# Kernel tuning notes

Measured on AMD Instinct MI355X. Metric: run time of the kernel, lower is better.

## Reference

```python
import jax, jax.numpy as jnp
import numpy as np

B, HF, WF = 4, 64, 64   # fine (output) resolution
HC, WC = 32, 32         # coarse resolution
CF = 256                # fine channels
CC = 256                # coarse channels (DCN input)
F = 256                 # filters
DG, K, KK = 8, 3, 9     # deformable groups, kernel
OFFS = DG * 2 * KK      # 144 offset channels
MASKS = DG * KK         # 72 mask channels
PAD = 1                 # 'same' padding for k=3, dil=1


def setup_inputs() -> dict:
    key = jax.random.key(0)
    ks = jax.random.split(key, 8)
    rn = lambda k, s, sc: jax.random.normal(k, s, jnp.float32) * sc
    return {
        "fine": rn(ks[0], (B, HF, WF, CF), 1.0),
        "coarse": rn(ks[1], (B, HC, WC, CC), 1.0),
        "fs_attn_w": rn(ks[2], (CF, CF), (2.0 / CF) ** 0.5),
        "fs_conv_w": rn(ks[3], (CF, F), (2.0 / CF) ** 0.5),
        "offset_w": rn(ks[4], (F + CC, 2 * F), (2.0 / (F + CC)) ** 0.5),
        "om_w": rn(ks[5], (K, K, 2 * F, OFFS + MASKS), 0.01),  # original is zero-init; small random for nontrivial offsets
        "om_b": jnp.zeros((OFFS + MASKS,), jnp.float32),
        "dcn_kernel": rn(ks[6], (KK * CC, F), 1.0 / np.sqrt(KK * CC)),
        "dcn_bias": jnp.zeros((F,), jnp.float32),
    }


def _dcn_columns(x, offset, mask):
    # x: [B,H,W,C]; offset: [B,H,W,DG,KK,2] (dy,dx); mask: [B,H,W,DG,KK]
    Bx, H, W, C = x.shape
    Cg = C // DG
    xg = x.reshape(Bx, H, W, DG, Cg)
    dt = x.dtype
    ky, kx = jnp.meshgrid(jnp.arange(K), jnp.arange(K), indexing="ij")
    tap_y = (ky.reshape(-1) - PAD).astype(dt)  # [KK]
    tap_x = (kx.reshape(-1) - PAD).astype(dt)
    # fractional sample positions, stride 1 / dilation 1
    py = (jnp.arange(H, dtype=dt)[None, :, None, None, None]
          + tap_y[None, None, None, None, :] + offset[..., 0])  # [B,H,W,DG,KK]
    px = (jnp.arange(W, dtype=dt)[None, None, :, None, None]
          + tap_x[None, None, None, None, :] + offset[..., 1])
    y0 = jnp.floor(py); x0 = jnp.floor(px)
    wy1 = py - y0; wx1 = px - x0
    wy0 = 1.0 - wy1; wx0 = 1.0 - wx1
    y0i = y0.astype(jnp.int32); x0i = x0.astype(jnp.int32)
    bi = jnp.arange(Bx).reshape(Bx, 1, 1, 1, 1)
    gi = jnp.arange(DG).reshape(1, 1, 1, DG, 1)

    def gather(yi, xi):
        valid = (yi >= 0) & (yi < H) & (xi >= 0) & (xi < W)
        yc = jnp.clip(yi, 0, H - 1)
        xc = jnp.clip(xi, 0, W - 1)
        v = xg[bi, yc, xc, gi]  # [B,H,W,DG,KK,Cg]
        return v * valid.astype(dt)[..., None]

    val = (gather(y0i, x0i) * (wy0 * wx0)[..., None]
           + gather(y0i, x0i + 1) * (wy0 * wx1)[..., None]
           + gather(y0i + 1, x0i) * (wy1 * wx0)[..., None]
           + gather(y0i + 1, x0i + 1) * (wy1 * wx1)[..., None])
    val = val * mask[..., None]  # modulation
    # column layout: tap-major, then channel (g*Cg + cg), matching kernel [KK*C, F]
    cols = jnp.transpose(val, (0, 1, 2, 4, 3, 5)).reshape(Bx, H, W, KK * C)
    return cols


def reference(fine, coarse, fs_attn_w, fs_conv_w, offset_w, om_w, om_b,
              dcn_kernel, dcn_bias):
    # 1) upsample coarse to fine resolution (half-pixel bilinear)
    coarse_up = jax.image.resize(coarse, (B, HF, WF, CC), "bilinear")
    # 2) FeatureSelection: GAP -> 1x1 sigmoid attention -> x*(a+1) -> 1x1 conv
    gap = jnp.mean(fine, axis=(1, 2), keepdims=True)
    attn = jax.nn.sigmoid(jnp.einsum("bhwc,cd->bhwd", gap, fs_attn_w))
    fine_cal = jnp.einsum("bhwc,cf->bhwf", fine * (attn + 1.0), fs_conv_w)
    # 3) offset features from concat(fine_cal, 2*coarse_up) via 1x1 conv
    fc = jnp.concatenate([fine_cal, coarse_up * 2.0], axis=-1)
    align = jnp.einsum("bhwc,cf->bhwf", fc, offset_w)
    # 4) DCNv2: offset/mask predictor conv (3x3 same)
    om = jax.lax.conv_general_dilated(
        align, om_w, (1, 1), "SAME",
        dimension_numbers=("NHWC", "HWIO", "NHWC")) + om_b
    offset = om[..., :OFFS].reshape(B, HF, WF, DG, KK, 2)
    mask = (jax.nn.sigmoid(om[..., OFFS:]) * 2.0).reshape(B, HF, WF, DG, KK)
    # 5) modulated deformable im2col + matmul + bias
    cols = _dcn_columns(coarse_up, offset, mask)
    out = cols @ dcn_kernel + dcn_bias
    # 6) activation + residual with selected fine features
    return jax.nn.relu(out) + fine_cal
```

## Files before the change

### kernel.cpp

```cpp
#include <hip/hip_runtime.h>
#include <hip/hip_bf16.h>

using u16 = unsigned short;
typedef __attribute__((ext_vector_type(8))) short short8;
typedef __attribute__((ext_vector_type(4))) float floatx4;
typedef __attribute__((ext_vector_type(4))) unsigned int uintx4;

__device__ __forceinline__ float b2f(u16 u) {
    union { unsigned int i; float f; } v; v.i = ((unsigned int)u) << 16; return v.f;
}
__device__ __forceinline__ u16 f2b(float f) {
    __hip_bfloat16 h = __float2bfloat16(f);
    u16 u; __builtin_memcpy(&u, &h, sizeof(u)); return u;
}


__global__ __launch_bounds__(256) void k_pre(const float* __restrict__ fine,
                                             const float* __restrict__ coarse,
                                             const float* __restrict__ fsw,
                                             const float* __restrict__ Wk,
                                             const float* __restrict__ omw,
                                             float* __restrict__ gap,
                                             u16* __restrict__ fcu,
                                             u16* __restrict__ wb0,
                                             u16* __restrict__ wkt,
                                             u16* __restrict__ bomw) {
    int bxg = blockIdx.x;
    int tid = threadIdx.x;
    if (bxg < 128) {
        int b = bxg >> 5, chunk = bxg & 31, c = tid;
        const float* p = fine + ((size_t)b * 4096 + (size_t)chunk * 128) * 256 + c;
        float s = 0.f;
        for (int i = 0; i < 128; i++) s += p[(size_t)i * 256];
        atomicAdd(&gap[b * 256 + c], s);
        return;
    }
    if (bxg < 640) {
        int p = (bxg - 128) * 32 + (tid >> 3);
        int ch = (tid & 7) * 32;
        int b = p >> 12, y = (p & 4095) >> 6, x = p & 63;
        float sy = fminf(fmaxf(0.5f * y - 0.25f, 0.0f), 31.0f);
        float sx = fminf(fmaxf(0.5f * x - 0.25f, 0.0f), 31.0f);
        int y0 = (int)floorf(sy); float wy = sy - (float)y0; int y1 = min(y0 + 1, 31);
        int x0 = (int)floorf(sx); float wx = sx - (float)x0; int x1 = min(x0 + 1, 31);
        float w00 = (1.f - wy) * (1.f - wx), w01 = (1.f - wy) * wx;
        float w10 = wy * (1.f - wx), w11 = wy * wx;
        const float* c00 = coarse + ((size_t)((b * 32 + y0) * 32 + x0)) * 256 + ch;
        const float* c01 = coarse + ((size_t)((b * 32 + y0) * 32 + x1)) * 256 + ch;
        const float* c10 = coarse + ((size_t)((b * 32 + y1) * 32 + x0)) * 256 + ch;
        const float* c11 = coarse + ((size_t)((b * 32 + y1) * 32 + x1)) * 256 + ch;
        u16* dst = fcu + (size_t)p * 512 + 256 + ch;
        #pragma unroll
        for (int k = 0; k < 4; k++) {
            float4 a0 = *(const float4*)(c00 + k * 8), a1v = *(const float4*)(c00 + k * 8 + 4);
            float4 b0 = *(const float4*)(c01 + k * 8), b1v = *(const float4*)(c01 + k * 8 + 4);
            float4 g0 = *(const float4*)(c10 + k * 8), g1 = *(const float4*)(c10 + k * 8 + 4);
            float4 d0 = *(const float4*)(c11 + k * 8), d1 = *(const float4*)(c11 + k * 8 + 4);
            u16 o[8] = {
                f2b(w00 * a0.x + w01 * b0.x + w10 * g0.x + w11 * d0.x),
                f2b(w00 * a0.y + w01 * b0.y + w10 * g0.y + w11 * d0.y),
                f2b(w00 * a0.z + w01 * b0.z + w10 * g0.z + w11 * d0.z),
                f2b(w00 * a0.w + w01 * b0.w + w10 * g0.w + w11 * d0.w),
                f2b(w00 * a1v.x + w01 * b1v.x + w10 * g1.x + w11 * d1.x),
                f2b(w00 * a1v.y + w01 * b1v.y + w10 * g1.y + w11 * d1.y),
                f2b(w00 * a1v.z + w01 * b1v.z + w10 * g1.z + w11 * d1.z),
                f2b(w00 * a1v.w + w01 * b1v.w + w10 * g1.w + w11 * d1.w)};
            uint4 ov; __builtin_memcpy(&ov, o, 16);
            *(uint4*)(dst + k * 8) = ov;
        }
        return;
    }
    int bx = bxg - 640;
    if (bx < 32) {
        int idx = bx * 256 + tid;
        int lane = idx & 63, nt = (idx >> 6) & 15, ks = idx >> 10;
        int n = nt * 16 + (lane & 15);
        int k0 = ks * 32 + (lane >> 4) * 8;
        u16 tmp[8];
        #pragma unroll
        for (int j = 0; j < 8; j++) tmp[j] = f2b(fsw[(size_t)(k0 + j) * 256 + n]);
        uint4 v; __builtin_memcpy(&v, tmp, 16);
        *(uint4*)(wb0 + (size_t)idx * 8) = v;
    } else if (bx < 320) {
        int idx = (bx - 32) * 256 + tid;
        int lane = idx & 63, nt = (idx >> 6) & 15, ks = idx >> 10;
        int n = nt * 16 + (lane & 15);
        int k0 = ks * 32 + (lane >> 4) * 8;
        u16 tmp[8];
        #pragma unroll
        for (int j = 0; j < 8; j++) tmp[j] = f2b(Wk[(size_t)(k0 + j) * 256 + n]);
        uint4 v; __builtin_memcpy(&v, tmp, 16);
        *(uint4*)(wkt + (size_t)idx * 8) = v;
    } else {
        int idx = (bx - 320) * 256 + tid;
        int lane = idx & 63, nt = (idx >> 6) & 15, ks = (idx >> 10) & 15, t = idx >> 14;
        int n = nt * 16 + (lane & 15);
        int f0 = ks * 32 + (lane >> 4) * 8;
        u16 tmp[8];
        #pragma unroll
        for (int j = 0; j < 8; j++)
            tmp[j] = (n < 216) ? f2b(omw[((size_t)t * 512 + f0 + j) * 216 + n]) : (u16)0;
        uint4 v; __builtin_memcpy(&v, tmp, 16);
        *(uint4*)(bomw + (size_t)idx * 8) = v;
    }
}

__global__ __launch_bounds__(256) void k_aw(const float* __restrict__ gap,
                                            const float* __restrict__ attw,
                                            float* __restrict__ a1,
                                            const float* __restrict__ ow,
                                            const u16* __restrict__ bomw,
                                            u16* __restrict__ wtf) {
    __shared__ u16 cols[32 * 520];
    int bxg = blockIdx.x;
    int tid = threadIdx.x;
    if (bxg < 4) {
        int b = bxg, d = tid;
        float s = 0.f;
        for (int c = 0; c < 256; c++) s += gap[b * 256 + c] * attw[c * 256 + d];
        s *= (1.0f / 4096.0f);
        a1[b * 256 + d] = 1.0f + 1.0f / (1.0f + expf(-s));
        return;
    }
    int i = bxg - 4;
    int c0 = (i & 15) * 32, t = i >> 4;
    int lane = tid & 63, wid = tid >> 6;
    int r = lane & 15, quad = lane >> 4;
    int sp = tid >> 3, f0 = (tid & 7) * 64;
    {
        const float* src = ow + (size_t)(c0 + sp) * 512 + f0;
        u16* dst = &cols[sp * 520 + f0];
        #pragma unroll
        for (int k = 0; k < 8; k++) {
            float4 v0 = *(const float4*)(src + k * 8);
            float4 v1 = *(const float4*)(src + k * 8 + 4);
            u16 o[8] = {f2b(v0.x), f2b(v0.y), f2b(v0.z), f2b(v0.w),
                        f2b(v1.x), f2b(v1.y), f2b(v1.z), f2b(v1.w)};
            uint4 ov; __builtin_memcpy(&ov, o, 16);
            *(uint4*)(dst + k * 8) = ov;
        }
    }
    __syncthreads();
    floatx4 acc[2][4];
    #pragma unroll
    for (int ii = 0; ii < 2; ii++)
        #pragma unroll
        for (int j = 0; j < 4; j++) acc[ii][j] = (floatx4){0.f, 0.f, 0.f, 0.f};
    #pragma unroll
    for (int ks = 0; ks < 16; ks++) {
        short8 a0 = *(const short8*)&cols[r * 520 + ks * 32 + quad * 8];
        short8 a1v = *(const short8*)&cols[(16 + r) * 520 + ks * 32 + quad * 8];
        const u16* bp = bomw + (((size_t)(t * 16 + ks) * 16 + wid * 4) * 64 + lane) * 8;
        short8 b0 = *(const short8*)(bp);
        short8 b1 = *(const short8*)(bp + 512);
        short8 b2 = *(const short8*)(bp + 1024);
        short8 b3 = *(const short8*)(bp + 1536);
        acc[0][0] = __builtin_amdgcn_mfma_f32_16x16x32_bf16(a0, b0, acc[0][0], 0, 0, 0);
        acc[0][1] = __builtin_amdgcn_mfma_f32_16x16x32_bf16(a0, b1, acc[0][1], 0, 0, 0);
        acc[0][2] = __builtin_amdgcn_mfma_f32_16x16x32_bf16(a0, b2, acc[0][2], 0, 0, 0);
        acc[0][3] = __builtin_amdgcn_mfma_f32_16x16x32_bf16(a0, b3, acc[0][3], 0, 0, 0);
        acc[1][0] = __builtin_amdgcn_mfma_f32_16x16x32_bf16(a1v, b0, acc[1][0], 0, 0, 0);
        acc[1][1] = __builtin_amdgcn_mfma_f32_16x16x32_bf16(a1v, b1, acc[1][1], 0, 0, 0);
        acc[1][2] = __builtin_amdgcn_mfma_f32_16x16x32_bf16(a1v, b2, acc[1][2], 0, 0, 0);
        acc[1][3] = __builtin_amdgcn_mfma_f32_16x16x32_bf16(a1v, b3, acc[1][3], 0, 0, 0);
    }
    #pragma unroll
    for (int mt = 0; mt < 2; mt++) {
        #pragma unroll
        for (int nt = 0; nt < 4; nt++) {
            int n = wid * 64 + nt * 16 + r;
            #pragma unroll
            for (int reg = 0; reg < 4; reg++) {
                int c = c0 + mt * 16 + quad * 4 + reg;
                float sc = (c >= 256) ? 2.0f : 1.0f;
                size_t addr = (((size_t)(t * 16 + (c >> 5)) * 16 + (n >> 4)) * 64
                               + ((c >> 3) & 3) * 16 + (n & 15)) * 8 + (c & 7);
                wtf[addr] = f2b(acc[mt][nt][reg] * sc);
            }
        }
    }
}

__global__ __launch_bounds__(256) void k_g0(const float* __restrict__ fine,
                                            const float* __restrict__ a1,
                                            const u16* __restrict__ wb,
                                            u16* __restrict__ fcu) {
    __shared__ u16 cols[32 * 264];
    int tid = threadIdx.x;
    int m0 = blockIdx.x * 32;
    int lane = tid & 63, wid = tid >> 6;
    int r = lane & 15, quad = lane >> 4;
    int sp = tid >> 3, coff = (tid & 7) * 32;
    int row = m0 + sp;
    int b = row >> 12;
    {
        const float* src = fine + (size_t)row * 256 + coff;
        const float* ap = a1 + b * 256 + coff;
        u16* dst = &cols[sp * 264 + coff];
        #pragma unroll
        for (int ch = 0; ch < 4; ch++) {
            float4 v0 = *(const float4*)(src + ch * 8);
            float4 v1 = *(const float4*)(src + ch * 8 + 4);
            float4 s0 = *(const float4*)(ap + ch * 8);
            float4 s1 = *(const float4*)(ap + ch * 8 + 4);
            u16 o[8] = {f2b(v0.x * s0.x), f2b(v0.y * s0.y), f2b(v0.z * s0.z), f2b(v0.w * s0.w),
                        f2b(v1.x * s1.x), f2b(v1.y * s1.y), f2b(v1.z * s1.z), f2b(v1.w * s1.w)};
            uint4 ov; __builtin_memcpy(&ov, o, 16);
            *(uint4*)(dst + ch * 8) = ov;
        }
    }
    __syncthreads();
    floatx4 acc[2][4];
    #pragma unroll
    for (int i = 0; i < 2; i++)
        #pragma unroll
        for (int j = 0; j < 4; j++) acc[i][j] = (floatx4){0.f, 0.f, 0.f, 0.f};
    #pragma unroll
    for (int ks = 0; ks < 8; ks++) {
        short8 a0 = *(const short8*)&cols[r * 264 + ks * 32 + quad * 8];
        short8 a1v = *(const short8*)&cols[(16 + r) * 264 + ks * 32 + quad * 8];
        const u16* bp = wb + (((size_t)ks * 16 + wid * 4) * 64 + lane) * 8;
        short8 b0 = *(const short8*)(bp);
        short8 b1 = *(const short8*)(bp + 512);
        short8 b2 = *(const short8*)(bp + 1024);
        short8 b3 = *(const short8*)(bp + 1536);
        acc[0][0] = __builtin_amdgcn_mfma_f32_16x16x32_bf16(a0, b0, acc[0][0], 0, 0, 0);
        acc[0][1] = __builtin_amdgcn_mfma_f32_16x16x32_bf16(a0, b1, acc[0][1], 0, 0, 0);
        acc[0][2] = __builtin_amdgcn_mfma_f32_16x16x32_bf16(a0, b2, acc[0][2], 0, 0, 0);
        acc[0][3] = __builtin_amdgcn_mfma_f32_16x16x32_bf16(a0, b3, acc[0][3], 0, 0, 0);
        acc[1][0] = __builtin_amdgcn_mfma_f32_16x16x32_bf16(a1v, b0, acc[1][0], 0, 0, 0);
        acc[1][1] = __builtin_amdgcn_mfma_f32_16x16x32_bf16(a1v, b1, acc[1][1], 0, 0, 0);
        acc[1][2] = __builtin_amdgcn_mfma_f32_16x16x32_bf16(a1v, b2, acc[1][2], 0, 0, 0);
        acc[1][3] = __builtin_amdgcn_mfma_f32_16x16x32_bf16(a1v, b3, acc[1][3], 0, 0, 0);
    }
    #pragma unroll
    for (int mt = 0; mt < 2; mt++)
        #pragma unroll
        for (int nt = 0; nt < 4; nt++) {
            int f = wid * 64 + nt * 16 + r;
            #pragma unroll
            for (int reg = 0; reg < 4; reg++) {
                int pp = m0 + mt * 16 + quad * 4 + reg;
                fcu[(size_t)pp * 512 + f] = f2b(acc[mt][nt][reg]);
            }
        }
}

__global__ __launch_bounds__(256, 4) void k_conv(const u16* __restrict__ fcu,
                                                 const u16* __restrict__ wtf,
                                                 const float* __restrict__ bias,
                                                 float* __restrict__ om) {
    __shared__ u16 halo[2][60 * 40];
    int tid = threadIdx.x;
    int bx = blockIdx.x;
    int xcd = bx & 7, i = bx >> 3;
    int prow4 = xcd * 8 + (i >> 4);
    int pcol = (i >> 1) & 7;
    int ns = i & 1;
    int b = prow4 >> 4;
    int py0 = (prow4 & 15) * 4, px0 = pcol * 8;
    int n0 = ns * 128;
    int lane = tid & 63, wid = tid >> 6;
    int r = lane & 15, quad = lane >> 4;

    int pix0 = tid >> 2, q80 = tid & 3;
    int hy0 = pix0 / 10, hx0 = pix0 - hy0 * 10;
    int gy0 = py0 - 1 + hy0, gx0 = px0 - 1 + hx0;
    bool act0 = pix0 < 60;
    bool in0 = act0 && gy0 >= 0 && gy0 < 64 && gx0 >= 0 && gx0 < 64;
    const u16* gs0 = fcu + ((size_t)((b * 64 + min(max(gy0, 0), 63)) * 64 + min(max(gx0, 0), 63))) * 512 + q80 * 8;
    int ld0 = pix0 * 40 + q80 * 8;

    floatx4 acc[2][2];
    #pragma unroll
    for (int a = 0; a < 2; a++)
        #pragma unroll
        for (int c = 0; c < 2; c++) acc[a][c] = (floatx4){0.f, 0.f, 0.f, 0.f};

    {
        uint4 v0 = make_uint4(0, 0, 0, 0);
        if (in0) v0 = *(const uint4*)(gs0);
        if (act0) *(uint4*)&halo[0][ld0] = v0;
    }
    __syncthreads();

    for (int cq = 0; cq < 16; cq++) {
        int cur = cq & 1;
        const u16* hb = &halo[cur][0];
        short8 Bp[2][2];
        #pragma unroll
        for (int d = 0; d < 2; d++) {
            const u16* bp = wtf + (((size_t)(d * 16 + cq) * 16 + ns * 8 + wid * 2) * 64 + lane) * 8;
            Bp[d][0] = *(const short8*)(bp);
            Bp[d][1] = *(const short8*)(bp + 512);
        }
        uint4 v0 = make_uint4(0, 0, 0, 0);
        #pragma unroll
        for (int t = 0; t < 7; t++) {
            int d = t & 1;
            short8 b0 = Bp[d][0], b1 = Bp[d][1];
            const u16* bp = wtf + (((size_t)((t + 2) * 16 + cq) * 16 + ns * 8 + wid * 2) * 64 + lane) * 8;
            Bp[d][0] = *(const short8*)(bp);
            Bp[d][1] = *(const short8*)(bp + 512);
            int dy = t / 3 - 1, dx = t - (t / 3) * 3 - 1;
            short8 a[2];
            #pragma unroll
            for (int mt = 0; mt < 2; mt++) {
                int m = mt * 16 + r;
                int hy = (m >> 3) + 1 + dy, hx = (m & 7) + 1 + dx;
                a[mt] = *(const short8*)&hb[(hy * 10 + hx) * 40 + quad * 8];
            }
            #pragma unroll
            for (int mt = 0; mt < 2; mt++) {
                acc[mt][0] = __builtin_amdgcn_mfma_f32_16x16x32_bf16(a[mt], b0, acc[mt][0], 0, 0, 0);
                acc[mt][1] = __builtin_amdgcn_mfma_f32_16x16x32_bf16(a[mt], b1, acc[mt][1], 0, 0, 0);
            }
        }
        if (cq < 15) {
            if (in0) v0 = *(const uint4*)(gs0 + (cq + 1) * 32);
        }
        #pragma unroll
        for (int t = 7; t < 9; t++) {
            int d = t & 1;
            short8 b0 = Bp[d][0], b1 = Bp[d][1];
            int dy = t / 3 - 1, dx = t - (t / 3) * 3 - 1;
            short8 a[2];
            #pragma unroll
            for (int mt = 0; mt < 2; mt++) {
                int m = mt * 16 + r;
                int hy = (m >> 3) + 1 + dy, hx = (m & 7) + 1 + dx;
                a[mt] = *(const short8*)&hb[(hy * 10 + hx) * 40 + quad * 8];
            }
            #pragma unroll
            for (int mt = 0; mt < 2; mt++) {
                acc[mt][0] = __builtin_amdgcn_mfma_f32_16x16x32_bf16(a[mt], b0, acc[mt][0], 0, 0, 0);
                acc[mt][1] = __builtin_amdgcn_mfma_f32_16x16x32_bf16(a[mt], b1, acc[mt][1], 0, 0, 0);
            }
        }
        if (cq < 15) {
            if (act0) *(uint4*)&halo[cur ^ 1][ld0] = v0;
        }
        __syncthreads();
    }
    #pragma unroll
    for (int nt = 0; nt < 2; nt++) {
        int n = n0 + wid * 32 + nt * 16 + r;
        if (n < 216) {
            float bv = bias[n];
            #pragma unroll
            for (int mt = 0; mt < 2; mt++) {
                #pragma unroll
                for (int reg = 0; reg < 4; reg++) {
                    int m = mt * 16 + quad * 4 + reg;
                    int gyy = py0 + (m >> 3), gxx = px0 + (m & 7);
                    size_t pix = (size_t)((b * 64 + gyy) * 64 + gxx);
                    om[pix * 216 + n] = acc[mt][nt][reg] + bv;
                }
            }
        }
    }
}

#define KEEP8(G) asm volatile("" :: "v"((G)[0][0]), "v"((G)[0][1]), \
                                    "v"((G)[1][0]), "v"((G)[1][1]), \
                                    "v"((G)[2][0]), "v"((G)[2][1]), \
                                    "v"((G)[3][0]), "v"((G)[3][1]))

__device__ __forceinline__ void dcn_addr1(int g3, int tl, int y, int xs, int ch0,
                                          float oy, float ox, float mlog,
                                          float w[4], int ofs[4]) {
    int dy = g3 - 1, dx = tl - 1;
    float mk = 2.0f / (1.0f + expf(-mlog));
    float py = (float)(y + dy) + oy;
    float px = (float)(xs + dx) + ox;
    float fy = floorf(py), fx = floorf(px);
    int iy = (int)fy, ix = (int)fx;
    float wy1 = py - fy, wx1 = px - fx;
    float wy0 = 1.f - wy1, wx0 = 1.f - wx1;
    bool y0in = iy >= 0 && iy < 64, y1in = iy >= -1 && iy < 63;
    bool x0in = ix >= 0 && ix < 64, x1in = ix >= -1 && ix < 63;
    w[0] = (y0in && x0in) ? wy0 * wx0 * mk : 0.f;
    w[1] = (y0in && x1in) ? wy0 * wx1 * mk : 0.f;
    w[2] = (y1in && x0in) ? wy1 * wx0 * mk : 0.f;
    w[3] = (y1in && x1in) ? wy1 * wx1 * mk : 0.f;
    int iy0 = min(max(iy, 0), 63), iy1 = min(max(iy + 1, 0), 63);
    int ix0 = min(max(ix, 0), 63), ix1 = min(max(ix + 1, 0), 63);
    ofs[0] = (iy0 * 64 + ix0) * 512 + ch0;
    ofs[1] = (iy0 * 64 + ix1) * 512 + ch0;
    ofs[2] = (iy1 * 64 + ix0) * 512 + ch0;
    ofs[3] = (iy1 * 64 + ix1) * 512 + ch0;
}

__device__ __forceinline__ void dcn_issue(uintx4 G[4][2], const u16* __restrict__ cub,
                                          const int ofs[4]) {
    #pragma unroll
    for (int c = 0; c < 4; c++) {
        const u16* p = cub + ofs[c];
        G[c][0] = *(const uintx4*)(p);
        G[c][1] = *(const uintx4*)(p + 8);
    }
}

__device__ __forceinline__ void dcn_blend(const uintx4 G[4][2], const float w[4],
                                          u16* __restrict__ dst) {
    #pragma unroll
    for (int k = 0; k < 2; k++) {
        const u16* q0 = (const u16*)&G[0][k];
        const u16* q1 = (const u16*)&G[1][k];
        const u16* q2 = (const u16*)&G[2][k];
        const u16* q3 = (const u16*)&G[3][k];
        u16 o[8];
        #pragma unroll
        for (int j = 0; j < 8; j++) {
            float v = w[0] * b2f(q0[j]) + w[1] * b2f(q1[j])
                    + w[2] * b2f(q2[j]) + w[3] * b2f(q3[j]);
            o[j] = f2b(v);
        }
        uint4 ov; __builtin_memcpy(&ov, o, 16);
        *(uint4*)(dst + k * 8) = ov;
    }
}

__global__ __launch_bounds__(512, 2) void k_dcn(const u16* __restrict__ fcu,
                                                const float* __restrict__ om,
                                                const u16* __restrict__ bfr,
                                                const float* __restrict__ bias,
                                                float* __restrict__ out) {
    __shared__ u16 cols[32 * 776];
    int tid = threadIdx.x;
    int bx = blockIdx.x;
    int xcd = bx & 7, i = bx >> 3;
    int grow = xcd * 32 + (i >> 1);
    int p0 = grow * 64 + (i & 1) * 32;
    int b = p0 >> 12;
    int y = (p0 & 4095) >> 6;
    int x0 = p0 & 63;
    int lane = tid & 63, wid = tid >> 6;
    int r = lane & 15, quad = lane >> 4;
    int sp = tid >> 4;
    int sgh = tid & 15;
    int g = sgh >> 1, h = sgh & 1;
    int ch0 = g * 32 + h * 16;
    int pix = p0 + sp;
    int xs = x0 + sp;
    const u16* cub = fcu + ((size_t)b * 4096) * 512 + 256;
    const float* omp = om + (size_t)pix * 216;
    u16* mydst = &cols[0] + sp * 776 + ch0;

    floatx4 acc[2][2];
    #pragma unroll
    for (int a = 0; a < 2; a++)
        #pragma unroll
        for (int c = 0; c < 2; c++) acc[a][c] = (floatx4){0.f, 0.f, 0.f, 0.f};

    #pragma unroll
    for (int g3 = 0; g3 < 3; g3++) {
        float oy[3], ox[3], mm[3];
        #pragma unroll
        for (int tl = 0; tl < 3; tl++) {
            int t = g3 * 3 + tl;
            oy[tl] = omp[g * 18 + 2 * t];
            ox[tl] = omp[g * 18 + 2 * t + 1];
            mm[tl] = omp[144 + g * 9 + t];
        }
        float w0[4], w1[4], w2[4];
        int o0[4], o1[4], o2[4];
        uintx4 G0[4][2], G1[4][2], G2[4][2];
        dcn_addr1(g3, 0, y, xs, ch0, oy[0], ox[0], mm[0], w0, o0);
        dcn_issue(G0, cub, o0);
        dcn_addr1(g3, 1, y, xs, ch0, oy[1], ox[1], mm[1], w1, o1);
        dcn_issue(G1, cub, o1);
        __builtin_amdgcn_sched_barrier(0);
        KEEP8(G0);
        __builtin_amdgcn_sched_barrier(0);
        dcn_blend(G0, w0, mydst + 0 * 256);
        dcn_addr1(g3, 2, y, xs, ch0, oy[2], ox[2], mm[2], w2, o2);
        dcn_issue(G2, cub, o2);
        __builtin_amdgcn_sched_barrier(0);
        KEEP8(G1);
        __builtin_amdgcn_sched_barrier(0);
        dcn_blend(G1, w1, mydst + 1 * 256);
        KEEP8(G2);
        __builtin_amdgcn_sched_barrier(0);
        dcn_blend(G2, w2, mydst + 2 * 256);
        __syncthreads();
        short8 Bb[4][2];
        #pragma unroll
        for (int d = 0; d < 4; d++) {
            const u16* bp = bfr + (((size_t)(g3 * 24 + d) * 16 + wid * 2) * 64 + lane) * 8;
            Bb[d][0] = *(const short8*)(bp);
            Bb[d][1] = *(const short8*)(bp + 512);
        }
        #pragma unroll
        for (int ksl = 0; ksl < 24; ksl++) {
            int d = ksl & 3;
            short8 b0 = Bb[d][0], b1 = Bb[d][1];
            if (ksl + 4 < 24) {
                const u16* bp = bfr + (((size_t)(g3 * 24 + ksl + 4) * 16 + wid * 2) * 64 + lane) * 8;
                Bb[d][0] = *(const short8*)(bp);
                Bb[d][1] = *(const short8*)(bp + 512);
            }
            short8 a0 = *(const short8*)&cols[r * 776 + ksl * 32 + quad * 8];
            short8 a1 = *(const short8*)&cols[(16 + r) * 776 + ksl * 32 + quad * 8];
            acc[0][0] = __builtin_amdgcn_mfma_f32_16x16x32_bf16(a0, b0, acc[0][0], 0, 0, 0);
            acc[0][1] = __builtin_amdgcn_mfma_f32_16x16x32_bf16(a0, b1, acc[0][1], 0, 0, 0);
            acc[1][0] = __builtin_amdgcn_mfma_f32_16x16x32_bf16(a1, b0, acc[1][0], 0, 0, 0);
            acc[1][1] = __builtin_amdgcn_mfma_f32_16x16x32_bf16(a1, b1, acc[1][1], 0, 0, 0);
        }
        __syncthreads();
    }
    #pragma unroll
    for (int mt = 0; mt < 2; mt++) {
        #pragma unroll
        for (int nt = 0; nt < 2; nt++) {
            int f = wid * 32 + nt * 16 + r;
            float bv = bias[f];
            #pragma unroll
            for (int reg = 0; reg < 4; reg++) {
                int pp = p0 + mt * 16 + quad * 4 + reg;
                float fcv = b2f(fcu[(size_t)pp * 512 + f]);
                out[(size_t)pp * 256 + f] = fmaxf(acc[mt][nt][reg] + bv, 0.f) + fcv;
            }
        }
    }
}

extern "C" void kernel_launch(void* const* d_in, const int* in_sizes, int n_in,
                              void* d_out, int out_size, void* d_ws, size_t ws_size,
                              hipStream_t stream) {
    const float* fine       = (const float*)d_in[0];
    const float* coarse     = (const float*)d_in[1];
    const float* fs_attn_w  = (const float*)d_in[2];
    const float* fs_conv_w  = (const float*)d_in[3];
    const float* offset_w   = (const float*)d_in[4];
    const float* om_w       = (const float*)d_in[5];
    const float* om_b       = (const float*)d_in[6];
    const float* dcn_kernel = (const float*)d_in[7];
    const float* dcn_bias   = (const float*)d_in[8];
    float* out = (float*)d_out;

    char* ws = (char*)d_ws;
    size_t off = 0;
    float* gap = (float*)(ws + off); off += 4096;
    float* a1  = (float*)(ws + off); off += 4096;
    u16*   fcu = (u16*)(ws + off);   off += 16777216ull;
    float* om  = (float*)(ws + off); off += 14155776ull;
    u16*   wtf = (u16*)(ws + off);   off += 2359296ull;
    u16*   wkt = (u16*)(ws + off);   off += 1179648ull;
    u16*   wb0 = (u16*)(ws + off);   off += 131072ull;
    u16*   bomw = (u16*)(ws + off);  off += 2359296ull;

    hipMemsetAsync(gap, 0, 4 * 256 * sizeof(float), stream);
    k_pre<<<1536, 256, 0, stream>>>(fine, coarse, fs_conv_w, dcn_kernel, om_w,
                                    gap, fcu, wb0, wkt, bomw);
    k_aw<<<148, 256, 0, stream>>>(gap, fs_attn_w, a1, offset_w, bomw, wtf);
    k_g0<<<512, 256, 0, stream>>>(fine, a1, wb0, fcu);
    k_conv<<<1024, 256, 0, stream>>>(fcu, wtf, om_b, om);
    k_dcn<<<512, 512, 0, stream>>>(fcu, om, wkt, dcn_bias, out);
}
```

Baseline: 210.3 us.

## Merge attention, fine GEMM and weight-transform kernels; replace gap atomics with partial sums

```diff
diff --git a/kernel.cpp b/kernel.cpp
--- a/kernel.cpp
+++ b/kernel.cpp
@@ -20,7 +20,7 @@
                                              const float* __restrict__ fsw,
                                              const float* __restrict__ Wk,
                                              const float* __restrict__ omw,
-                                             float* __restrict__ gap,
+                                             float* __restrict__ gap_part,
                                              u16* __restrict__ fcu,
                                              u16* __restrict__ wb0,
                                              u16* __restrict__ wkt,
@@ -32,7 +32,7 @@
         const float* p = fine + ((size_t)b * 4096 + (size_t)chunk * 128) * 256 + c;
         float s = 0.f;
         for (int i = 0; i < 128; i++) s += p[(size_t)i * 256];
-        atomicAdd(&gap[b * 256 + c], s);
+        gap_part[(size_t)bxg * 256 + c] = s;
         return;
     }
     if (bxg < 640) {
@@ -105,27 +105,99 @@
     }
 }
 
-__global__ __launch_bounds__(256) void k_aw(const float* __restrict__ gap,
-                                            const float* __restrict__ attw,
-                                            float* __restrict__ a1,
-                                            const float* __restrict__ ow,
-                                            const u16* __restrict__ bomw,
-                                            u16* __restrict__ wtf) {
-    __shared__ u16 cols[32 * 520];
+__global__ __launch_bounds__(256) void k_mid(const float* __restrict__ fine,
+                                             const float* __restrict__ gap_part,
+                                             const float* __restrict__ attw,
+                                             const u16* __restrict__ wb,
+                                             u16* __restrict__ fcu,
+                                             const float* __restrict__ ow,
+                                             const u16* __restrict__ bomw,
+                                             u16* __restrict__ wtf) {
+    __shared__ u16 smem[32 * 520];
     int bxg = blockIdx.x;
     int tid = threadIdx.x;
-    if (bxg < 4) {
-        int b = bxg, d = tid;
-        float s = 0.f;
-        for (int c = 0; c < 256; c++) s += gap[b * 256 + c] * attw[c * 256 + d];
-        s *= (1.0f / 4096.0f);
-        a1[b * 256 + d] = 1.0f + 1.0f / (1.0f + expf(-s));
-        return;
-    }
-    int i = bxg - 4;
-    int c0 = (i & 15) * 32, t = i >> 4;
     int lane = tid & 63, wid = tid >> 6;
     int r = lane & 15, quad = lane >> 4;
+    if (bxg < 512) {
+        u16* cols = smem;
+        float* gaprow = (float*)(smem + 32 * 264);
+        float* a1row  = (float*)(smem + 32 * 264 + 512);
+        int m0 = bxg * 32;
+        int b = m0 >> 12;
+        {
+            const float* gp = gap_part + (size_t)b * 32 * 256 + tid;
+            float gsum = 0.f;
+            #pragma unroll
+            for (int k = 0; k < 32; k++) gsum += gp[(size_t)k * 256];
+            gaprow[tid] = gsum;
+        }
+        __syncthreads();
+        {
+            const float* wcol = attw + tid;
+            float s = 0.f;
+            #pragma unroll 8
+            for (int c = 0; c < 256; c++) s += gaprow[c] * wcol[(size_t)c * 256];
+            s *= (1.0f / 4096.0f);
+            a1row[tid] = 1.0f + 1.0f / (1.0f + expf(-s));
+        }
+        __syncthreads();
+        int sp = tid >> 3, coff = (tid & 7) * 32;
+        int row = m0 + sp;
+        {
+            const float* src = fine + (size_t)row * 256 + coff;
+            u16* dst = &cols[sp * 264 + coff];
+            #pragma unroll
+            for (int ch = 0; ch < 4; ch++) {
+                float4 v0 = *(const float4*)(src + ch * 8);
+                float4 v1 = *(const float4*)(src + ch * 8 + 4);
+                float4 s0 = *(const float4*)(&a1row[coff + ch * 8]);
+                float4 s1 = *(const float4*)(&a1row[coff + ch * 8 + 4]);
+                u16 o[8] = {f2b(v0.x * s0.x), f2b(v0.y * s0.y), f2b(v0.z * s0.z), f2b(v0.w * s0.w),
+                            f2b(v1.x * s1.x), f2b(v1.y * s1.y), f2b(v1.z * s1.z), f2b(v1.w * s1.w)};
+                uint4 ov; __builtin_memcpy(&ov, o, 16);
+                *(uint4*)(dst + ch * 8) = ov;
+            }
+        }
+        __syncthreads();
+        floatx4 acc[2][4];
+        #pragma unroll
+        for (int i = 0; i < 2; i++)
+            #pragma unroll
+            for (int j = 0; j < 4; j++) acc[i][j] = (floatx4){0.f, 0.f, 0.f, 0.f};
+        #pragma unroll
+        for (int ks = 0; ks < 8; ks++) {
+            short8 a0 = *(const short8*)&cols[r * 264 + ks * 32 + quad * 8];
+            short8 a1v = *(const short8*)&cols[(16 + r) * 264 + ks * 32 + quad * 8];
+            const u16* bp = wb + (((size_t)ks * 16 + wid * 4) * 64 + lane) * 8;
+            short8 b0 = *(const short8*)(bp);
+            short8 b1 = *(const short8*)(bp + 512);
+            short8 b2 = *(const short8*)(bp + 1024);
+            short8 b3 = *(const short8*)(bp + 1536);
+            acc[0][0] = __builtin_amdgcn_mfma_f32_16x16x32_bf16(a0, b0, acc[0][0], 0, 0, 0);
+            acc[0][1] = __builtin_amdgcn_mfma_f32_16x16x32_bf16(a0, b1, acc[0][1], 0, 0, 0);
+            acc[0][2] = __builtin_amdgcn_mfma_f32_16x16x32_bf16(a0, b2, acc[0][2], 0, 0, 0);
+            acc[0][3] = __builtin_amdgcn_mfma_f32_16x16x32_bf16(a0, b3, acc[0][3], 0, 0, 0);
+            acc[1][0] = __builtin_amdgcn_mfma_f32_16x16x32_bf16(a1v, b0, acc[1][0], 0, 0, 0);
+            acc[1][1] = __builtin_amdgcn_mfma_f32_16x16x32_bf16(a1v, b1, acc[1][1], 0, 0, 0);
+            acc[1][2] = __builtin_amdgcn_mfma_f32_16x16x32_bf16(a1v, b2, acc[1][2], 0, 0, 0);
+            acc[1][3] = __builtin_amdgcn_mfma_f32_16x16x32_bf16(a1v, b3, acc[1][3], 0, 0, 0);
+        }
+        #pragma unroll
+        for (int mt = 0; mt < 2; mt++)
+            #pragma unroll
+            for (int nt = 0; nt < 4; nt++) {
+                int f = wid * 64 + nt * 16 + r;
+                #pragma unroll
+                for (int reg = 0; reg < 4; reg++) {
+                    int pp = m0 + mt * 16 + quad * 4 + reg;
+                    fcu[(size_t)pp * 512 + f] = f2b(acc[mt][nt][reg]);
+                }
+            }
+        return;
+    }
+    int i = bxg - 512;
+    int c0 = (i & 15) * 32, t = i >> 4;
+    u16* cols = smem;
     int sp = tid >> 3, f0 = (tid & 7) * 64;
     {
         const float* src = ow + (size_t)(c0 + sp) * 512 + f0;
@@ -179,71 +251,6 @@
             }
         }
     }
-}
-
-__global__ __launch_bounds__(256) void k_g0(const float* __restrict__ fine,
-                                            const float* __restrict__ a1,
-                                            const u16* __restrict__ wb,
-                                            u16* __restrict__ fcu) {
-    __shared__ u16 cols[32 * 264];
-    int tid = threadIdx.x;
-    int m0 = blockIdx.x * 32;
-    int lane = tid & 63, wid = tid >> 6;
-    int r = lane & 15, quad = lane >> 4;
-    int sp = tid >> 3, coff = (tid & 7) * 32;
-    int row = m0 + sp;
-    int b = row >> 12;
-    {
-        const float* src = fine + (size_t)row * 256 + coff;
-        const float* ap = a1 + b * 256 + coff;
-        u16* dst = &cols[sp * 264 + coff];
-        #pragma unroll
-        for (int ch = 0; ch < 4; ch++) {
-            float4 v0 = *(const float4*)(src + ch * 8);
-            float4 v1 = *(const float4*)(src + ch * 8 + 4);
-            float4 s0 = *(const float4*)(ap + ch * 8);
-            float4 s1 = *(const float4*)(ap + ch * 8 + 4);
-            u16 o[8] = {f2b(v0.x * s0.x), f2b(v0.y * s0.y), f2b(v0.z * s0.z), f2b(v0.w * s0.w),
-                        f2b(v1.x * s1.x), f2b(v1.y * s1.y), f2b(v1.z * s1.z), f2b(v1.w * s1.w)};
-            uint4 ov; __builtin_memcpy(&ov, o, 16);
-            *(uint4*)(dst + ch * 8) = ov;
-        }
-    }
-    __syncthreads();
-    floatx4 acc[2][4];
-    #pragma unroll
-    for (int i = 0; i < 2; i++)
-        #pragma unroll
-        for (int j = 0; j < 4; j++) acc[i][j] = (floatx4){0.f, 0.f, 0.f, 0.f};
-    #pragma unroll
-    for (int ks = 0; ks < 8; ks++) {
-        short8 a0 = *(const short8*)&cols[r * 264 + ks * 32 + quad * 8];
-        short8 a1v = *(const short8*)&cols[(16 + r) * 264 + ks * 32 + quad * 8];
-        const u16* bp = wb + (((size_t)ks * 16 + wid * 4) * 64 + lane) * 8;
-        short8 b0 = *(const short8*)(bp);
-        short8 b1 = *(const short8*)(bp + 512);
-        short8 b2 = *(const short8*)(bp + 1024);
-        short8 b3 = *(const short8*)(bp + 1536);
-        acc[0][0] = __builtin_amdgcn_mfma_f32_16x16x32_bf16(a0, b0, acc[0][0], 0, 0, 0);
-        acc[0][1] = __builtin_amdgcn_mfma_f32_16x16x32_bf16(a0, b1, acc[0][1], 0, 0, 0);
-        acc[0][2] = __builtin_amdgcn_mfma_f32_16x16x32_bf16(a0, b2, acc[0][2], 0, 0, 0);
-        acc[0][3] = __builtin_amdgcn_mfma_f32_16x16x32_bf16(a0, b3, acc[0][3], 0, 0, 0);
-        acc[1][0] = __builtin_amdgcn_mfma_f32_16x16x32_bf16(a1v, b0, acc[1][0], 0, 0, 0);
-        acc[1][1] = __builtin_amdgcn_mfma_f32_16x16x32_bf16(a1v, b1, acc[1][1], 0, 0, 0);
-        acc[1][2] = __builtin_amdgcn_mfma_f32_16x16x32_bf16(a1v, b2, acc[1][2], 0, 0, 0);
-        acc[1][3] = __builtin_amdgcn_mfma_f32_16x16x32_bf16(a1v, b3, acc[1][3], 0, 0, 0);
-    }
-    #pragma unroll
-    for (int mt = 0; mt < 2; mt++)
-        #pragma unroll
-        for (int nt = 0; nt < 4; nt++) {
-            int f = wid * 64 + nt * 16 + r;
-            #pragma unroll
-            for (int reg = 0; reg < 4; reg++) {
-                int pp = m0 + mt * 16 + quad * 4 + reg;
-                fcu[(size_t)pp * 512 + f] = f2b(acc[mt][nt][reg]);
-            }
-        }
 }
 
 __global__ __launch_bounds__(256, 4) void k_conv(const u16* __restrict__ fcu,
@@ -541,8 +548,7 @@
 
     char* ws = (char*)d_ws;
     size_t off = 0;
-    float* gap = (float*)(ws + off); off += 4096;
-    float* a1  = (float*)(ws + off); off += 4096;
+    float* gap_part = (float*)(ws + off); off += 131072;
     u16*   fcu = (u16*)(ws + off);   off += 16777216ull;
     float* om  = (float*)(ws + off); off += 14155776ull;
     u16*   wtf = (u16*)(ws + off);   off += 2359296ull;
@@ -550,11 +556,10 @@
     u16*   wb0 = (u16*)(ws + off);   off += 131072ull;
     u16*   bomw = (u16*)(ws + off);  off += 2359296ull;
 
-    hipMemsetAsync(gap, 0, 4 * 256 * sizeof(float), stream);
     k_pre<<<1536, 256, 0, stream>>>(fine, coarse, fs_conv_w, dcn_kernel, om_w,
-                                    gap, fcu, wb0, wkt, bomw);
-    k_aw<<<148, 256, 0, stream>>>(gap, fs_attn_w, a1, offset_w, bomw, wtf);
-    k_g0<<<512, 256, 0, stream>>>(fine, a1, wb0, fcu);
+                                    gap_part, fcu, wb0, wkt, bomw);
+    k_mid<<<656, 256, 0, stream>>>(fine, gap_part, fs_attn_w, wb0, fcu,
+                                   offset_w, bomw, wtf);
     k_conv<<<1024, 256, 0, stream>>>(fcu, wtf, om_b, om);
     k_dcn<<<512, 512, 0, stream>>>(fcu, om, wkt, dcn_bias, out);
 }
```

Result: faster. 205.6 us (median of 2 runs) (-2.3%).
